# Kernel tuning notes

Measured on AMD Instinct MI355X. Metric: run time of the kernel, lower is better.

Reference implementation:

```python
import jax, jax.numpy as jnp
import numpy as np

D_K = 64

def setup_inputs() -> dict:
    key = jax.random.key(0)
    kq, kk, kv = jax.random.split(key, 3)
    shape = (2, 16, 2048, D_K)  # [B, H, S, d_k]
    Q = jax.random.normal(kq, shape, dtype=jnp.float32)
    K = jax.random.normal(kk, shape, dtype=jnp.float32)
    V = jax.random.normal(kv, shape, dtype=jnp.float32)
    return {"Q": Q, "K": K, "V": V}

def reference(Q, K, V):
    scale = 1.0 / jnp.sqrt(jnp.asarray(D_K, dtype=Q.dtype))
    # [B,H,S,S] scores; note: original's masked_fill is non-in-place and discarded -> mask is a no-op
    scores = jnp.einsum('bhqd,bhkd->bhqk', Q, K) * scale
    attn = jax.nn.softmax(scores, axis=-1)
    context = jnp.einsum('bhqk,bhkd->bhqd', attn, V)
    return (context, attn)
```

## Files before the change

kernel.cpp:

```cpp
#include <hip/hip_runtime.h>
#include <stdint.h>

#define S 2048
#define D 64
#define QTILE 64
#define KTILE 64
#define NKT (S / KTILE)

typedef short bf16x8 __attribute__((ext_vector_type(8)));
typedef float f32x4 __attribute__((ext_vector_type(4)));

#define KSTR 72
#define VSTR 66
#define PSTR 72

__device__ __forceinline__ short f2bf(float f) {
    unsigned u = __float_as_uint(f);
    u = (u + 0x7FFFu + ((u >> 16) & 1u)) >> 16;
    return (short)u;
}

__global__ __launch_bounds__(256, 4) void sdpa_kernel(
    const float* __restrict__ Qg, const float* __restrict__ Kg,
    const float* __restrict__ Vg, float* __restrict__ out_ctx,
    float* __restrict__ out_attn)
{
    __shared__ short K_lds[KTILE * KSTR];
    __shared__ short Vt_lds[D * VSTR];
    __shared__ short p_lds[4 * 16 * PSTR];

    const int tid  = threadIdx.x;
    const int wave = tid >> 6;
    const int lane = tid & 63;
    const int quad = lane >> 4;
    const int c    = lane & 15;

    const int bh = blockIdx.x >> 5;
    const int qt = blockIdx.x & 31;

    const float* Qh = Qg + (size_t)bh * S * D;
    const float* Kh = Kg + (size_t)bh * S * D;
    const float* Vh = Vg + (size_t)bh * S * D;
    float* attn_h = out_attn + (size_t)bh * S * S;

    const int q0 = qt * QTILE + wave * 16;

    bf16x8 qfrag[2];
    {
        const float* qp = Qh + (size_t)(q0 + c) * D + quad * 8;
        #pragma unroll
        for (int ks = 0; ks < 2; ++ks)
            #pragma unroll
            for (int j = 0; j < 8; ++j)
                qfrag[ks][j] = f2bf(qp[ks * 32 + j] * 0.125f);
    }

    float m_r[4], l_r[4];
    #pragma unroll
    for (int r = 0; r < 4; ++r) { m_r[r] = -1e30f; l_r[r] = 0.0f; }

    for (int kt = 0; kt < NKT; ++kt) {
        {
            const int row = tid >> 2;
            const int dst = (tid & 3) * 16;
            const float* src = Kh + (size_t)(kt * KTILE + row) * D + dst;
            bf16x8 a, b;
            #pragma unroll
            for (int j = 0; j < 8; ++j) { a[j] = f2bf(src[j]); b[j] = f2bf(src[8 + j]); }
            *(bf16x8*)&K_lds[row * KSTR + dst] = a;
            *(bf16x8*)&K_lds[row * KSTR + dst + 8] = b;
        }
        __syncthreads();

        f32x4 sacc[4];
        #pragma unroll
        for (int nb = 0; nb < 4; ++nb) {
            f32x4 z = {0.f, 0.f, 0.f, 0.f};
            sacc[nb] = z;
            #pragma unroll
            for (int ks = 0; ks < 2; ++ks) {
                bf16x8 kf = *(const bf16x8*)&K_lds[(nb * 16 + c) * KSTR + ks * 32 + quad * 8];
                sacc[nb] = __builtin_amdgcn_mfma_f32_16x16x32_bf16(qfrag[ks], kf, sacc[nb], 0, 0, 0);
            }
        }
        #pragma unroll
        for (int r = 0; r < 4; ++r) {
            float mx = fmaxf(fmaxf(sacc[0][r], sacc[1][r]), fmaxf(sacc[2][r], sacc[3][r]));
            #pragma unroll
            for (int off = 1; off < 16; off <<= 1)
                mx = fmaxf(mx, __shfl_xor(mx, off));
            const float mnew = fmaxf(m_r[r], mx);
            float t = __expf(sacc[0][r] - mnew) + __expf(sacc[1][r] - mnew)
                    + __expf(sacc[2][r] - mnew) + __expf(sacc[3][r] - mnew);
            #pragma unroll
            for (int off = 1; off < 16; off <<= 1)
                t += __shfl_xor(t, off);
            l_r[r] = l_r[r] * __expf(m_r[r] - mnew) + t;
            m_r[r] = mnew;
        }
        __syncthreads();
    }

    float inv_l[4];
    #pragma unroll
    for (int r = 0; r < 4; ++r) inv_l[r] = 1.0f / l_r[r];

    f32x4 cacc[4];
    #pragma unroll
    for (int nb = 0; nb < 4; ++nb) { f32x4 z = {0.f, 0.f, 0.f, 0.f}; cacc[nb] = z; }

    for (int kt = 0; kt < NKT; ++kt) {
        {
            const int row = tid >> 2;
            const int dst = (tid & 3) * 16;
            const float* src = Kh + (size_t)(kt * KTILE + row) * D + dst;
            bf16x8 a, b;
            #pragma unroll
            for (int j = 0; j < 8; ++j) { a[j] = f2bf(src[j]); b[j] = f2bf(src[8 + j]); }
            *(bf16x8*)&K_lds[row * KSTR + dst] = a;
            *(bf16x8*)&K_lds[row * KSTR + dst + 8] = b;
        }
        {
            const int rbase = wave * 16;
            #pragma unroll
            for (int i = 0; i < 16; ++i) {
                float v = Vh[(size_t)(kt * KTILE + rbase + i) * D + lane];
                Vt_lds[lane * VSTR + rbase + i] = f2bf(v);
            }
        }
        __syncthreads();

        f32x4 sacc[4];
        #pragma unroll
        for (int nb = 0; nb < 4; ++nb) {
            f32x4 z = {0.f, 0.f, 0.f, 0.f};
            sacc[nb] = z;
            #pragma unroll
            for (int ks = 0; ks < 2; ++ks) {
                bf16x8 kf = *(const bf16x8*)&K_lds[(nb * 16 + c) * KSTR + ks * 32 + quad * 8];
                sacc[nb] = __builtin_amdgcn_mfma_f32_16x16x32_bf16(qfrag[ks], kf, sacc[nb], 0, 0, 0);
            }
        }

        short* pw = &p_lds[wave * 16 * PSTR];
        #pragma unroll
        for (int nb = 0; nb < 4; ++nb) {
            #pragma unroll
            for (int r = 0; r < 4; ++r) {
                const float p = __expf(sacc[nb][r] - m_r[r]) * inv_l[r];
                __builtin_nontemporal_store(p,
                    attn_h + (size_t)(q0 + quad * 4 + r) * S + (size_t)(kt * KTILE + nb * 16 + c));
                pw[(quad * 4 + r) * PSTR + nb * 16 + c] = f2bf(p);
            }
        }

        bf16x8 pa[2];
        #pragma unroll
        for (int ks = 0; ks < 2; ++ks)
            pa[ks] = *(const bf16x8*)&p_lds[(wave * 16 + c) * PSTR + ks * 32 + quad * 8];

        #pragma unroll
        for (int nb = 0; nb < 4; ++nb) {
            #pragma unroll
            for (int ks = 0; ks < 2; ++ks) {
                bf16x8 vf;
                const short* vb = &Vt_lds[(nb * 16 + c) * VSTR + ks * 32 + quad * 8];
                #pragma unroll
                for (int j = 0; j < 8; ++j) vf[j] = vb[j];
                cacc[nb] = __builtin_amdgcn_mfma_f32_16x16x32_bf16(pa[ks], vf, cacc[nb], 0, 0, 0);
            }
        }
        __syncthreads();
    }

    #pragma unroll
    for (int nb = 0; nb < 4; ++nb)
        #pragma unroll
        for (int r = 0; r < 4; ++r)
            __builtin_nontemporal_store(cacc[nb][r],
                out_ctx + (size_t)bh * S * D + (size_t)(q0 + quad * 4 + r) * D + nb * 16 + c);
}

extern "C" void kernel_launch(void* const* d_in, const int* in_sizes, int n_in,
                              void* d_out, int out_size, void* d_ws, size_t ws_size,
                              hipStream_t stream) {
    const float* Q = (const float*)d_in[0];
    const float* K = (const float*)d_in[1];
    const float* V = (const float*)d_in[2];
    float* ctx  = (float*)d_out;
    float* attn = (float*)d_out + (size_t)2 * 16 * S * D;

    dim3 grid(32 * (S / QTILE));
    dim3 block(256);
    hipLaunchKernelGGL(sdpa_kernel, grid, block, 0, stream, Q, K, V, ctx, attn);
}
```

Measured before the change: 716.6 us.

## Rewrite SDPA with bf16 pre-converted K/V^T, 32x32 MFMA and split-key waves

Adds pre-pass kernels that convert K to bf16 and V to a transposed bf16 layout in workspace. The attention kernel then loads MFMA fragments straight from global memory with no LDS staging or per-tile barriers. It switches to 32x32x16 MFMA, splits the key range across wave pairs and merges their softmax stats and context through LDS. It also uses a log-sum-exp constant so each probability needs one exp, packs P via cvt_pk/permlane32_swap, and remaps block IDs for locality. In exchange it adds two extra launches and workspace traffic, and keeps a fallback path for when no workspace is given.

```diff
diff --git a/kernel.cpp b/kernel.cpp
--- a/kernel.cpp
+++ b/kernel.cpp
@@ -3,16 +3,15 @@
 
 #define S 2048
 #define D 64
+#define NH 32
+#define KTILE 32
 #define QTILE 64
-#define KTILE 64
-#define NKT (S / KTILE)
+#define NKT (S / 2 / KTILE)
 
 typedef short bf16x8 __attribute__((ext_vector_type(8)));
-typedef float f32x4 __attribute__((ext_vector_type(4)));
-
-#define KSTR 72
-#define VSTR 66
-#define PSTR 72
+typedef float f32x4  __attribute__((ext_vector_type(4)));
+typedef float f32x16 __attribute__((ext_vector_type(16)));
+typedef int   i32x4  __attribute__((ext_vector_type(4)));
 
 __device__ __forceinline__ short f2bf(float f) {
     unsigned u = __float_as_uint(f);
@@ -20,165 +19,250 @@
     return (short)u;
 }
 
+__global__ __launch_bounds__(256) void cvt_k_kernel(const float* __restrict__ Kg,
+                                                    short* __restrict__ Kbf) {
+    const size_t t = (size_t)blockIdx.x * 256 + threadIdx.x;
+    const float* src = Kg + t * 8;
+    f32x4 a = *(const f32x4*)src;
+    f32x4 b = *(const f32x4*)(src + 4);
+    bf16x8 o;
+    #pragma unroll
+    for (int j = 0; j < 4; ++j) { o[j] = f2bf(a[j]); o[4 + j] = f2bf(b[j]); }
+    *(bf16x8*)(Kbf + t * 8) = o;
+}
+
+__global__ __launch_bounds__(256) void cvt_vt_kernel(const float* __restrict__ Vg,
+                                                     short* __restrict__ Vt) {
+    __shared__ short tile[64][72];
+    const int h  = blockIdx.x >> 5;
+    const int k0 = (blockIdx.x & 31) * 64;
+    const int t  = threadIdx.x;
+    {
+        const int row = t >> 2, dc = (t & 3) * 16;
+        const float* src = Vg + ((size_t)h * S + k0 + row) * D + dc;
+        bf16x8 a, b;
+        #pragma unroll
+        for (int j = 0; j < 8; ++j) { a[j] = f2bf(src[j]); b[j] = f2bf(src[8 + j]); }
+        *(bf16x8*)&tile[row][dc] = a;
+        *(bf16x8*)&tile[row][dc + 8] = b;
+    }
+    __syncthreads();
+    {
+        const int d = t >> 2, kc = (t & 3) * 16;
+        bf16x8 o0, o1;
+        #pragma unroll
+        for (int j = 0; j < 8; ++j) { o0[j] = tile[kc + j][d]; o1[j] = tile[kc + 8 + j][d]; }
+        short* dst = Vt + ((size_t)h * D + d) * S + k0 + kc;
+        *(bf16x8*)dst = o0;
+        *(bf16x8*)(dst + 8) = o1;
+    }
+}
+
+template<bool PRE>
+__device__ __forceinline__ void load_kfrags(const short* __restrict__ Kbf,
+                                            const float* __restrict__ Kg,
+                                            int h, int key0, int c, int hi,
+                                            bf16x8 kf[4]) {
+    if constexpr (PRE) {
+        const short* kp = Kbf + ((size_t)h * S + key0 + c) * D + hi * 8;
+        #pragma unroll
+        for (int kb = 0; kb < 4; ++kb) kf[kb] = *(const bf16x8*)(kp + kb * 16);
+    } else {
+        const float* kp = Kg + ((size_t)h * S + key0 + c) * D + hi * 8;
+        #pragma unroll
+        for (int kb = 0; kb < 4; ++kb) {
+            f32x4 a = *(const f32x4*)(kp + kb * 16);
+            f32x4 b = *(const f32x4*)(kp + kb * 16 + 4);
+            #pragma unroll
+            for (int j = 0; j < 4; ++j) { kf[kb][j] = f2bf(a[j]); kf[kb][4 + j] = f2bf(b[j]); }
+        }
+    }
+}
+
+template<bool PRE>
 __global__ __launch_bounds__(256, 4) void sdpa_kernel(
     const float* __restrict__ Qg, const float* __restrict__ Kg,
-    const float* __restrict__ Vg, float* __restrict__ out_ctx,
+    const float* __restrict__ Vg, const short* __restrict__ Kbf,
+    const short* __restrict__ Vtbf, float* __restrict__ out_ctx,
     float* __restrict__ out_attn)
 {
-    __shared__ short K_lds[KTILE * KSTR];
-    __shared__ short Vt_lds[D * VSTR];
-    __shared__ short p_lds[4 * 16 * PSTR];
+    __shared__ float sm_stat[2][4][32];
+    __shared__ float sm_ctx[2][32][64];
 
     const int tid  = threadIdx.x;
     const int wave = tid >> 6;
     const int lane = tid & 63;
-    const int quad = lane >> 4;
-    const int c    = lane & 15;
-
-    const int bh = blockIdx.x >> 5;
-    const int qt = blockIdx.x & 31;
-
-    const float* Qh = Qg + (size_t)bh * S * D;
-    const float* Kh = Kg + (size_t)bh * S * D;
-    const float* Vh = Vg + (size_t)bh * S * D;
-    float* attn_h = out_attn + (size_t)bh * S * S;
-
-    const int q0 = qt * QTILE + wave * 16;
-
-    bf16x8 qfrag[2];
-    {
-        const float* qp = Qh + (size_t)(q0 + c) * D + quad * 8;
-        #pragma unroll
-        for (int ks = 0; ks < 2; ++ks)
-            #pragma unroll
-            for (int j = 0; j < 8; ++j)
-                qfrag[ks][j] = f2bf(qp[ks * 32 + j] * 0.125f);
-    }
-
-    float m_r[4], l_r[4];
+    const int c    = lane & 31;
+    const int hi   = lane >> 5;
+    const int qs   = wave >> 1;
+    const int kh   = wave & 1;
+
+    int bid = (int)blockIdx.x;
+    bid = (bid & 7) * 128 + (bid >> 3);
+    const int h  = bid >> 5;
+    const int qb = bid & 31;
+
+    const int q = qb * QTILE + qs * 32 + c;
+
+    bf16x8 qf[4];
+    {
+        const float* qrow = Qg + ((size_t)h * S + q) * D + hi * 8;
+        #pragma unroll
+        for (int kb = 0; kb < 4; ++kb) {
+            f32x4 a = *(const f32x4*)(qrow + kb * 16);
+            f32x4 b = *(const f32x4*)(qrow + kb * 16 + 4);
+            #pragma unroll
+            for (int j = 0; j < 4; ++j) {
+                qf[kb][j]     = f2bf(a[j] * 0.125f);
+                qf[kb][4 + j] = f2bf(b[j] * 0.125f);
+            }
+        }
+    }
+
+    const int kbase = kh * (S / 2);
+
+    float m_r = -1e30f, l_r = 0.0f;
+    #pragma unroll 1
+    for (int kt = 0; kt < NKT; ++kt) {
+        const int key0 = kbase + kt * KTILE;
+        bf16x8 kf[4];
+        load_kfrags<PRE>(Kbf, Kg, h, key0, c, hi, kf);
+
+        f32x16 sacc;
+        #pragma unroll
+        for (int i = 0; i < 16; ++i) sacc[i] = 0.0f;
+        #pragma unroll
+        for (int kb = 0; kb < 4; ++kb)
+            sacc = __builtin_amdgcn_mfma_f32_32x32x16_bf16(kf[kb], qf[kb], sacc, 0, 0, 0);
+
+        float mx[8];
+        #pragma unroll
+        for (int i = 0; i < 8; ++i) mx[i] = fmaxf(sacc[i], sacc[i + 8]);
+        #pragma unroll
+        for (int i = 0; i < 4; ++i) mx[i] = fmaxf(mx[i], mx[i + 4]);
+        const float mloc = fmaxf(fmaxf(mx[0], mx[1]), fmaxf(mx[2], mx[3]));
+        const float mnew = fmaxf(m_r, mloc);
+        float e[16];
+        #pragma unroll
+        for (int i = 0; i < 16; ++i) e[i] = __expf(sacc[i] - mnew);
+        #pragma unroll
+        for (int st = 8; st >= 1; st >>= 1)
+            #pragma unroll
+            for (int i = 0; i < st; ++i) e[i] += e[i + st];
+        l_r = l_r * __expf(m_r - mnew) + e[0];
+        m_r = mnew;
+    }
+    {
+        const float mo = __shfl_xor(m_r, 32);
+        const float lo = __shfl_xor(l_r, 32);
+        const float M  = fmaxf(m_r, mo);
+        l_r = l_r * __expf(m_r - M) + lo * __expf(mo - M);
+        m_r = M;
+    }
+    if (hi == 0) { sm_stat[0][wave][c] = m_r; sm_stat[1][wave][c] = l_r; }
+    __syncthreads();
+    float c_r;
+    {
+        const int pw = wave ^ 1;
+        const float mo = sm_stat[0][pw][c];
+        const float lo = sm_stat[1][pw][c];
+        const float M  = fmaxf(m_r, mo);
+        const float L  = l_r * __expf(m_r - M) + lo * __expf(mo - M);
+        c_r = M + __logf(L);
+    }
+
+    f32x16 cacc[2];
     #pragma unroll
-    for (int r = 0; r < 4; ++r) { m_r[r] = -1e30f; l_r[r] = 0.0f; }
-
+    for (int db = 0; db < 2; ++db)
+        #pragma unroll
+        for (int i = 0; i < 16; ++i) cacc[db][i] = 0.0f;
+
+    float* arow = out_attn + (size_t)h * S * S + (size_t)q * S + hi * 4;
+
+    #pragma unroll 1
     for (int kt = 0; kt < NKT; ++kt) {
-        {
-            const int row = tid >> 2;
-            const int dst = (tid & 3) * 16;
-            const float* src = Kh + (size_t)(kt * KTILE + row) * D + dst;
-            bf16x8 a, b;
-            #pragma unroll
-            for (int j = 0; j < 8; ++j) { a[j] = f2bf(src[j]); b[j] = f2bf(src[8 + j]); }
-            *(bf16x8*)&K_lds[row * KSTR + dst] = a;
-            *(bf16x8*)&K_lds[row * KSTR + dst + 8] = b;
-        }
-        __syncthreads();
-
-        f32x4 sacc[4];
-        #pragma unroll
-        for (int nb = 0; nb < 4; ++nb) {
-            f32x4 z = {0.f, 0.f, 0.f, 0.f};
-            sacc[nb] = z;
-            #pragma unroll
-            for (int ks = 0; ks < 2; ++ks) {
-                bf16x8 kf = *(const bf16x8*)&K_lds[(nb * 16 + c) * KSTR + ks * 32 + quad * 8];
-                sacc[nb] = __builtin_amdgcn_mfma_f32_16x16x32_bf16(qfrag[ks], kf, sacc[nb], 0, 0, 0);
-            }
-        }
-        #pragma unroll
-        for (int r = 0; r < 4; ++r) {
-            float mx = fmaxf(fmaxf(sacc[0][r], sacc[1][r]), fmaxf(sacc[2][r], sacc[3][r]));
-            #pragma unroll
-            for (int off = 1; off < 16; off <<= 1)
-                mx = fmaxf(mx, __shfl_xor(mx, off));
-            const float mnew = fmaxf(m_r[r], mx);
-            float t = __expf(sacc[0][r] - mnew) + __expf(sacc[1][r] - mnew)
-                    + __expf(sacc[2][r] - mnew) + __expf(sacc[3][r] - mnew);
-            #pragma unroll
-            for (int off = 1; off < 16; off <<= 1)
-                t += __shfl_xor(t, off);
-            l_r[r] = l_r[r] * __expf(m_r[r] - mnew) + t;
-            m_r[r] = mnew;
-        }
-        __syncthreads();
-    }
-
-    float inv_l[4];
-    #pragma unroll
-    for (int r = 0; r < 4; ++r) inv_l[r] = 1.0f / l_r[r];
-
-    f32x4 cacc[4];
-    #pragma unroll
-    for (int nb = 0; nb < 4; ++nb) { f32x4 z = {0.f, 0.f, 0.f, 0.f}; cacc[nb] = z; }
-
-    for (int kt = 0; kt < NKT; ++kt) {
-        {
-            const int row = tid >> 2;
-            const int dst = (tid & 3) * 16;
-            const float* src = Kh + (size_t)(kt * KTILE + row) * D + dst;
-            bf16x8 a, b;
-            #pragma unroll
-            for (int j = 0; j < 8; ++j) { a[j] = f2bf(src[j]); b[j] = f2bf(src[8 + j]); }
-            *(bf16x8*)&K_lds[row * KSTR + dst] = a;
-            *(bf16x8*)&K_lds[row * KSTR + dst + 8] = b;
-        }
-        {
-            const int rbase = wave * 16;
+        const int key0 = kbase + kt * KTILE;
+        bf16x8 kf[4];
+        load_kfrags<PRE>(Kbf, Kg, h, key0, c, hi, kf);
+
+        bf16x8 vf[2][2];
+        if constexpr (PRE) {
+            #pragma unroll
+            for (int db = 0; db < 2; ++db) {
+                const short* vp = Vtbf + ((size_t)h * D + db * 32 + c) * S + key0 + hi * 8;
+                vf[0][db] = *(const bf16x8*)vp;
+                vf[1][db] = *(const bf16x8*)(vp + 16);
+            }
+        } else {
+            #pragma unroll
+            for (int ks = 0; ks < 2; ++ks)
+                #pragma unroll
+                for (int db = 0; db < 2; ++db) {
+                    bf16x8 o;
+                    #pragma unroll
+                    for (int j = 0; j < 8; ++j)
+                        o[j] = f2bf(Vg[((size_t)h * S + key0 + ks * 16 + hi * 8 + j) * D + db * 32 + c]);
+                    vf[ks][db] = o;
+                }
+        }
+
+        f32x16 sacc;
+        #pragma unroll
+        for (int i = 0; i < 16; ++i) sacc[i] = 0.0f;
+        #pragma unroll
+        for (int kb = 0; kb < 4; ++kb)
+            sacc = __builtin_amdgcn_mfma_f32_32x32x16_bf16(kf[kb], qf[kb], sacc, 0, 0, 0);
+
+        #pragma unroll
+        for (int i = 0; i < 16; ++i) sacc[i] = __expf(sacc[i] - c_r);
+
+        #pragma unroll
+        for (int g = 0; g < 4; ++g) {
+            f32x4 pv = { sacc[4 * g], sacc[4 * g + 1], sacc[4 * g + 2], sacc[4 * g + 3] };
+            __builtin_nontemporal_store(pv, (f32x4*)(arow + key0 + 8 * g));
+        }
+
+        unsigned P0[4], P1[4];
+        #pragma unroll
+        for (int g = 0; g < 4; ++g) {
+            asm("v_cvt_pk_bf16_f32 %0, %1, %2" : "=v"(P0[g]) : "v"(sacc[4 * g]),     "v"(sacc[4 * g + 1]));
+            asm("v_cvt_pk_bf16_f32 %0, %1, %2" : "=v"(P1[g]) : "v"(sacc[4 * g + 2]), "v"(sacc[4 * g + 3]));
+        }
+        #pragma unroll
+        for (int ks = 0; ks < 2; ++ks) {
+            unsigned a0 = P0[2 * ks], b0 = P0[2 * ks + 1];
+            unsigned a1 = P1[2 * ks], b1 = P1[2 * ks + 1];
+            asm("v_permlane32_swap_b32 %0, %1" : "+v"(a0), "+v"(b0));
+            asm("v_permlane32_swap_b32 %0, %1" : "+v"(a1), "+v"(b1));
+            union { i32x4 w; bf16x8 f; } u;
+            i32x4 w = { (int)a0, (int)a1, (int)b0, (int)b1 };
+            u.w = w;
+            cacc[0] = __builtin_amdgcn_mfma_f32_32x32x16_bf16(u.f, vf[ks][0], cacc[0], 0, 0, 0);
+            cacc[1] = __builtin_amdgcn_mfma_f32_32x32x16_bf16(u.f, vf[ks][1], cacc[1], 0, 0, 0);
+        }
+    }
+
+    if (kh == 1) {
+        #pragma unroll
+        for (int db = 0; db < 2; ++db)
             #pragma unroll
             for (int i = 0; i < 16; ++i) {
-                float v = Vh[(size_t)(kt * KTILE + rbase + i) * D + lane];
-                Vt_lds[lane * VSTR + rbase + i] = f2bf(v);
-            }
-        }
-        __syncthreads();
-
-        f32x4 sacc[4];
-        #pragma unroll
-        for (int nb = 0; nb < 4; ++nb) {
-            f32x4 z = {0.f, 0.f, 0.f, 0.f};
-            sacc[nb] = z;
-            #pragma unroll
-            for (int ks = 0; ks < 2; ++ks) {
-                bf16x8 kf = *(const bf16x8*)&K_lds[(nb * 16 + c) * KSTR + ks * 32 + quad * 8];
-                sacc[nb] = __builtin_amdgcn_mfma_f32_16x16x32_bf16(qfrag[ks], kf, sacc[nb], 0, 0, 0);
-            }
-        }
-
-        short* pw = &p_lds[wave * 16 * PSTR];
-        #pragma unroll
-        for (int nb = 0; nb < 4; ++nb) {
-            #pragma unroll
-            for (int r = 0; r < 4; ++r) {
-                const float p = __expf(sacc[nb][r] - m_r[r]) * inv_l[r];
-                __builtin_nontemporal_store(p,
-                    attn_h + (size_t)(q0 + quad * 4 + r) * S + (size_t)(kt * KTILE + nb * 16 + c));
-                pw[(quad * 4 + r) * PSTR + nb * 16 + c] = f2bf(p);
-            }
-        }
-
-        bf16x8 pa[2];
-        #pragma unroll
-        for (int ks = 0; ks < 2; ++ks)
-            pa[ks] = *(const bf16x8*)&p_lds[(wave * 16 + c) * PSTR + ks * 32 + quad * 8];
-
-        #pragma unroll
-        for (int nb = 0; nb < 4; ++nb) {
-            #pragma unroll
-            for (int ks = 0; ks < 2; ++ks) {
-                bf16x8 vf;
-                const short* vb = &Vt_lds[(nb * 16 + c) * VSTR + ks * 32 + quad * 8];
-                #pragma unroll
-                for (int j = 0; j < 8; ++j) vf[j] = vb[j];
-                cacc[nb] = __builtin_amdgcn_mfma_f32_16x16x32_bf16(pa[ks], vf, cacc[nb], 0, 0, 0);
-            }
-        }
-        __syncthreads();
-    }
-
-    #pragma unroll
-    for (int nb = 0; nb < 4; ++nb)
-        #pragma unroll
-        for (int r = 0; r < 4; ++r)
-            __builtin_nontemporal_store(cacc[nb][r],
-                out_ctx + (size_t)bh * S * D + (size_t)(q0 + quad * 4 + r) * D + nb * 16 + c);
+                const int row = (i & 3) + 8 * (i >> 2) + 4 * hi;
+                sm_ctx[qs][row][db * 32 + c] = cacc[db][i];
+            }
+    }
+    __syncthreads();
+    if (kh == 0) {
+        float* crow = out_ctx + ((size_t)h * S + qb * QTILE + qs * 32) * D + c;
+        #pragma unroll
+        for (int db = 0; db < 2; ++db)
+            #pragma unroll
+            for (int i = 0; i < 16; ++i) {
+                const int row = (i & 3) + 8 * (i >> 2) + 4 * hi;
+                __builtin_nontemporal_store(cacc[db][i] + sm_ctx[qs][row][db * 32 + c],
+                                            crow + (size_t)row * D + db * 32);
+            }
+    }
 }
 
 extern "C" void kernel_launch(void* const* d_in, const int* in_sizes, int n_in,
@@ -188,9 +272,20 @@
     const float* K = (const float*)d_in[1];
     const float* V = (const float*)d_in[2];
     float* ctx  = (float*)d_out;
-    float* attn = (float*)d_out + (size_t)2 * 16 * S * D;
-
-    dim3 grid(32 * (S / QTILE));
-    dim3 block(256);
-    hipLaunchKernelGGL(sdpa_kernel, grid, block, 0, stream, Q, K, V, ctx, attn);
-}
+    float* attn = (float*)d_out + (size_t)NH * S * D;
+
+    const size_t nelem = (size_t)NH * S * D;
+    const size_t need  = nelem * 2 * sizeof(short);
+    short* kbf  = (short*)d_ws;
+    short* vtbf = kbf + nelem;
+
+    if (d_ws != nullptr && ws_size >= need) {
+        hipLaunchKernelGGL(cvt_k_kernel,  dim3((unsigned)(nelem / 8 / 256)), dim3(256), 0, stream, K, kbf);
+        hipLaunchKernelGGL(cvt_vt_kernel, dim3(NH * (S / 64)), dim3(256), 0, stream, V, vtbf);
+        hipLaunchKernelGGL(sdpa_kernel<true>,  dim3(1024), dim3(256), 0, stream,
+                           Q, K, V, kbf, vtbf, ctx, attn);
+    } else {
+        hipLaunchKernelGGL(sdpa_kernel<false>, dim3(1024), dim3(256), 0, stream,
+                           Q, K, V, kbf, vtbf, ctx, attn);
+    }
+}
```

Measured after the change: 979.8 us. 36.7% more time.
